# Performance work log

Measured on AMD Instinct MI355X. Metric: run time of the kernel, lower is better.

Reference implementation:

```python
import jax, jax.numpy as jnp
import numpy as np

N_ATOMS = 8192
N_PAIR = 131072
F = 128
N_HEAD = 8
FH = F // N_HEAD            # 16
DEGREES = [1, 2, 3]
N_DEG = len(DEGREES)
REPEATS = np.array([2 * l + 1 for l in DEGREES])  # [3,5,7]
M_TOT = int(REPEATS.sum())  # 15
K_RBF = 32
H_FILT = 64
FILT_OUT = 2 * N_DEG * F    # 768


def setup_inputs() -> dict:
    key = jax.random.key(0)
    ks = jax.random.split(key, 12)
    x = jax.random.normal(ks[0], (N_ATOMS, F), dtype=jnp.float32)
    rbf_ij = jax.random.uniform(ks[1], (N_PAIR, K_RBF), dtype=jnp.float32)
    sph_ij = jax.random.normal(ks[2], (N_PAIR, M_TOT), dtype=jnp.float32)
    phi_r_cut = jax.random.uniform(ks[3], (N_PAIR,), dtype=jnp.float32)
    idx_i = jnp.sort(jax.random.randint(ks[4], (N_PAIR,), 0, N_ATOMS))
    idx_j = jax.random.randint(ks[5], (N_PAIR,), 0, N_ATOMS)
    pair_mask = jnp.ones((N_PAIR,), dtype=jnp.float32)
    # params (lecun-normal-ish scaling)
    W_Q = jax.random.normal(ks[6], (N_DEG, N_HEAD, FH, FH), dtype=jnp.float32) / np.sqrt(FH)
    W_K = jax.random.normal(ks[7], (N_DEG, N_HEAD, FH, FH), dtype=jnp.float32) / np.sqrt(FH)
    a = jax.random.normal(ks[8], (N_DEG, N_HEAD, 2 * FH), dtype=jnp.float32) / np.sqrt(2 * FH)
    mlp_w1 = jax.random.normal(ks[9], (K_RBF, H_FILT), dtype=jnp.float32) / np.sqrt(K_RBF)
    mlp_b1 = jnp.zeros((H_FILT,), dtype=jnp.float32)
    mlp_w2 = jax.random.normal(ks[10], (H_FILT, FILT_OUT), dtype=jnp.float32) / np.sqrt(H_FILT)
    mlp_b2 = jnp.zeros((FILT_OUT,), dtype=jnp.float32)
    return {"x": x, "rbf_ij": rbf_ij, "sph_ij": sph_ij, "phi_r_cut": phi_r_cut,
            "idx_i": idx_i, "idx_j": idx_j, "pair_mask": pair_mask,
            "W_Q": W_Q, "W_K": W_K, "a": a,
            "mlp_w1": mlp_w1, "mlp_b1": mlp_b1, "mlp_w2": mlp_w2, "mlp_b2": mlp_b2}


def reference(x, rbf_ij, sph_ij, phi_r_cut, idx_i, idx_j, pair_mask,
              W_Q, W_K, a, mlp_w1, mlp_b1, mlp_w2, mlp_b2):
    n = x.shape[0]
    x_head = x.reshape(n, N_HEAD, FH)                       # (n, h, fh)
    # per-atom, per-degree, per-head linear maps
    Q = jnp.einsum('dhij,nhj->ndhi', W_Q, x_head)           # (n, d, h, fh)
    K = jnp.einsum('dhij,nhj->ndhi', W_K, x_head)
    m4 = pair_mask[:, None, None, None]
    Q_i = Q[idx_i] * m4                                     # (p, d, h, fh)
    K_j = K[idx_j] * m4
    QK = jnp.concatenate((Q_i, K_j), axis=-1)               # (p, d, h, 2fh)
    # radial filter MLP
    h1 = jax.nn.silu(rbf_ij @ mlp_w1 + mlp_b1)
    W_ij = (h1 @ mlp_w2 + mlp_b2).reshape(-1, N_DEG, N_HEAD, 2 * FH)
    W_ij = W_ij * phi_r_cut[:, None, None, None]
    # attention logits (non-softmax)
    alpha = jnp.sum(QK * W_ij * a[None], axis=-1)           # (p, d, h)
    alpha = jnp.repeat(alpha, REPEATS, axis=1, total_repeat_length=M_TOT)  # (p, m, h)
    alpha = alpha / jnp.sqrt(jnp.float32(FH))               # att_scale
    # outer product with spherical harmonics + scatter
    x_j = x_head[idx_j] * pair_mask[:, None, None]          # (p, h, fh)
    z = alpha[..., None] * (sph_ij[:, :, None, None] * x_j[:, None, :, :])  # (p, m, h, fh)
    z = z.reshape(z.shape[0], M_TOT, F)                     # (p, m, F)
    return jax.ops.segment_sum(z, idx_i, num_segments=n)    # (n, m, F)
```

## Files before the change

### kernel.cpp

```cpp
#include <hip/hip_runtime.h>
#include <hip/hip_bf16.h>

#define N_ATOMS 8192
#define N_PAIR  131072
#define F       128
#define N_HEAD  8
#define FH      16
#define N_DEG   3
#define M_TOT   15
#define K_RBF   32
#define H_FILT  64
#define FILT_OUT 768
#define NDH     24
#define ATB     4

typedef __attribute__((ext_vector_type(8))) unsigned short u16x8;

__device__ __forceinline__ float bf2f(unsigned short u) {
    return __uint_as_float(((unsigned)u) << 16);
}
__device__ __forceinline__ unsigned short f2bfbits(float f) {
    __hip_bfloat16 b = __float2bfloat16(f);
    return *reinterpret_cast<unsigned short*>(&b);
}

__global__ void k_seg(const int* __restrict__ idx_i, int* __restrict__ row_start) {
    int p = blockIdx.x * 256 + threadIdx.x;
    if (p >= N_PAIR) return;
    int ii = idx_i[p];
    int prev = (p == 0) ? -1 : idx_i[p - 1];
    for (int a = prev + 1; a <= ii; ++a) row_start[a] = p;
    if (p == N_PAIR - 1) {
        for (int a = ii + 1; a <= N_ATOMS; ++a) row_start[a] = N_PAIR;
    }
}

__global__ void k_zero(int* __restrict__ counts, int* __restrict__ cnt2) {
    int t = blockIdx.x * 256 + threadIdx.x;
    if (t < N_ATOMS) { counts[t] = 0; cnt2[t] = 0; }
}

__global__ void k_hist(const int* __restrict__ idx_j, int* __restrict__ counts) {
    int p = blockIdx.x * 256 + threadIdx.x;
    if (p < N_PAIR) atomicAdd(&counts[idx_j[p]], 1);
}

__global__ __launch_bounds__(1024) void k_scan(const int* __restrict__ counts,
                                               int* __restrict__ offsets) {
    __shared__ int ts[1024];
    int tid = threadIdx.x;
    int base = tid * 8;
    int v[8]; int tot = 0;
    #pragma unroll
    for (int q = 0; q < 8; ++q) { v[q] = counts[base + q]; tot += v[q]; }
    ts[tid] = tot; __syncthreads();
    for (int off = 1; off < 1024; off <<= 1) {
        int t2 = (tid >= off) ? ts[tid - off] : 0;
        __syncthreads();
        ts[tid] += t2;
        __syncthreads();
    }
    int excl = ts[tid] - tot;
    #pragma unroll
    for (int q = 0; q < 8; ++q) { offsets[base + q] = excl; excl += v[q]; }
    if (tid == 1023) offsets[N_ATOMS] = ts[1023];
}

__global__ void k_place(const int* __restrict__ idx_j, const int* __restrict__ offsets,
                        int* __restrict__ cnt2, int* __restrict__ sorted,
                        int* __restrict__ rank) {
    int p = blockIdx.x * 256 + threadIdx.x;
    if (p < N_PAIR) {
        int j = idx_j[p];
        int pos = offsets[j] + atomicAdd(&cnt2[j], 1);
        sorted[pos] = p;
        rank[p] = pos;
    }
}

__global__ __launch_bounds__(256) void k_wc(
    const float* __restrict__ WQ, const float* __restrict__ WK,
    const float* __restrict__ avec, const float* __restrict__ W2,
    const float* __restrict__ b2,
    float* __restrict__ Wc, float* __restrict__ bc)
{
    int bx = blockIdx.x;
    int side = bx / NDH, dh = bx % NDH;
    int d = dh >> 3, h = dh & 7;
    int colbase = d * 256 + h * 32 + side * 16;
    const float* W = (side == 0) ? WQ : WK;
    __shared__ float w2s[64][16];
    __shared__ float ws[16][16];
    __shared__ float as[16];
    __shared__ float b2s[16];
    int tid = threadIdx.x;
    for (int e = tid; e < 64 * 16; e += 256)
        w2s[e >> 4][e & 15] = W2[(e >> 4) * FILT_OUT + colbase + (e & 15)];
    if (tid < 16 * 16) ws[tid >> 4][tid & 15] = W[((d * 8 + h) * 16) * 16 + tid];
    if (tid < 16) { as[tid] = avec[dh * 32 + side * 16 + tid]; b2s[tid] = b2[colbase + tid]; }
    __syncthreads();
    for (int o = tid; o < 64 * 16; o += 256) {
        int k = o >> 4, j = o & 15;
        float s = 0.f;
        #pragma unroll
        for (int c = 0; c < 16; ++c) s += w2s[k][c] * as[c] * ws[c][j];
        Wc[((size_t)bx * 64 + k) * 16 + j] = s;
    }
    if (tid < 16) {
        float s = 0.f;
        #pragma unroll
        for (int c = 0; c < 16; ++c) s += b2s[c] * as[c] * ws[c][tid];
        bc[bx * 16 + tid] = s;
    }
}

__global__ __launch_bounds__(256) void k_gfused(
    const float* __restrict__ x, const float* __restrict__ Wc,
    const float* __restrict__ bc,
    __hip_bfloat16* __restrict__ Gq, __hip_bfloat16* __restrict__ Gk,
    float* __restrict__ bq, float* __restrict__ bk)
{
    int bx = blockIdx.x;
    int by = blockIdx.y;
    int side = by / NDH, dh = by % NDH;
    int h = dh & 7;
    int n0 = bx * 64;
    __shared__ float xh[64][17];
    __shared__ float bcs[16];
    int tid = threadIdx.x;
    for (int e = tid; e < 64 * 16; e += 256)
        xh[e >> 4][e & 15] = x[(size_t)(n0 + (e >> 4)) * F + h * 16 + (e & 15)];
    if (tid < 16) bcs[tid] = bc[by * 16 + tid];
    int k = tid & 63, wv = tid >> 6;
    float wcr[16];
    const float* wp = Wc + ((size_t)by * 64 + k) * 16;
    #pragma unroll
    for (int j = 0; j < 16; ++j) wcr[j] = wp[j];
    __syncthreads();
    __hip_bfloat16* G = (side == 0) ? Gq : Gk;
    #pragma unroll 4
    for (int it = 0; it < 16; ++it) {
        int at = wv * 16 + it;
        float acc = 0.f;
        #pragma unroll
        for (int j = 0; j < 16; ++j) acc += wcr[j] * xh[at][j];
        G[(size_t)(n0 + at) * 1536 + dh * 64 + k] = __float2bfloat16(acc);
    }
    if (tid < 64) {
        float* B = (side == 0) ? bq : bk;
        float s = 0.f;
        #pragma unroll
        for (int j = 0; j < 16; ++j) s += bcs[j] * xh[tid][j];
        B[(n0 + tid) * NDH + dh] = s;
    }
}

__global__ __launch_bounds__(256) void k_h1(
    const float* __restrict__ rbf, const float* __restrict__ W1,
    const float* __restrict__ b1, unsigned short* __restrict__ h1)
{
    __shared__ float w1s[K_RBF][H_FILT];
    __shared__ float b1s[H_FILT];
    __shared__ float rbfs[64][33];
    int tid = threadIdx.x;
    int p0 = blockIdx.x * 64;
    for (int e = tid; e < K_RBF * H_FILT; e += 256) w1s[e >> 6][e & 63] = W1[e];
    if (tid < H_FILT) b1s[tid] = b1[tid];
    for (int e = tid; e < 64 * K_RBF; e += 256)
        rbfs[e >> 5][e & 31] = rbf[(size_t)p0 * K_RBF + e];
    __syncthreads();
    int pp = tid >> 2;
    int kbase = (tid & 3) * 16;
    float acc[16];
    #pragma unroll
    for (int q = 0; q < 16; ++q) acc[q] = b1s[kbase + q];
    for (int c = 0; c < K_RBF; ++c) {
        float r = rbfs[pp][c];
        #pragma unroll
        for (int q = 0; q < 16; ++q) acc[q] += r * w1s[c][kbase + q];
    }
    u16x8 o0, o1;
    #pragma unroll
    for (int q = 0; q < 8; ++q) {
        float s0 = acc[q];     o0[q] = f2bfbits(s0 / (1.f + __expf(-s0)));
        float s1 = acc[q + 8]; o1[q] = f2bfbits(s1 / (1.f + __expf(-s1)));
    }
    unsigned short* hp = h1 + (size_t)(p0 + pp) * 64 + kbase;
    *reinterpret_cast<u16x8*>(hp) = o0;
    *reinterpret_cast<u16x8*>(hp + 8) = o1;
}

__global__ __launch_bounds__(256) void k_alphak2(
    const int* __restrict__ sorted, const int* __restrict__ idx_j,
    const unsigned short* __restrict__ h1,
    const __hip_bfloat16* __restrict__ Gk, const float* __restrict__ bk,
    unsigned short* __restrict__ alphaKs)
{
    __shared__ unsigned short h1s[64][64];
    __shared__ float als[64][24];
    __shared__ int ps[64];
    __shared__ int js[64];
    int tid = threadIdx.x;
    int c0 = blockIdx.x * 64;
    if (tid < 64) {
        int pid = sorted[c0 + tid];
        ps[tid] = pid;
        js[tid] = idx_j[pid];
    }
    __syncthreads();
    for (int e = tid; e < 64 * 8; e += 256) {
        int slot = e >> 3, seg = e & 7;
        *reinterpret_cast<u16x8*>(&h1s[slot][seg * 8]) =
            *reinterpret_cast<const u16x8*>(h1 + (size_t)ps[slot] * 64 + seg * 8);
    }
    __syncthreads();
    const unsigned short* GkU = reinterpret_cast<const unsigned short*>(Gk);
    int seg = tid & 7;
    #pragma unroll 4
    for (int t = 0; t < 48; ++t) {
        int task = t * 256 + tid;
        int dhslot = task >> 3;
        int slot = dhslot / 24;
        int dh = dhslot - slot * 24;
        const unsigned short* g = GkU + (size_t)js[slot] * 1536 + dh * 64 + seg * 8;
        u16x8 gv = *reinterpret_cast<const u16x8*>(g);
        u16x8 hv = *reinterpret_cast<const u16x8*>(&h1s[slot][seg * 8]);
        float p = 0.f;
        #pragma unroll
        for (int v = 0; v < 8; ++v) p += bf2f(gv[v]) * bf2f(hv[v]);
        p += __shfl_xor(p, 1);
        p += __shfl_xor(p, 2);
        p += __shfl_xor(p, 4);
        if (seg == 0) als[slot][dh] = p;
    }
    __syncthreads();
    for (int e = tid; e < 64 * 24; e += 256) {
        int slot = e / 24, dh = e - slot * 24;
        float val = als[slot][dh] + bk[js[slot] * NDH + dh];
        alphaKs[(size_t)c0 * 24 + e] = f2bfbits(val);
    }
}

__global__ __launch_bounds__(256) void k_alphaA2(
    const int* __restrict__ idx_i, const int* __restrict__ rank,
    const float* __restrict__ phi, const float* __restrict__ mask,
    const unsigned short* __restrict__ h1,
    const __hip_bfloat16* __restrict__ Gq, const float* __restrict__ bq,
    const unsigned short* __restrict__ alphaKs,
    float* __restrict__ alphaF)
{
    __shared__ unsigned short h1s[64][64];
    __shared__ float als[64][24];
    __shared__ int is[64];
    __shared__ int rks[64];
    __shared__ float pms[64];
    int tid = threadIdx.x;
    int p0 = blockIdx.x * 64;
    if (tid < 64) {
        int p = p0 + tid;
        is[tid] = idx_i[p];
        rks[tid] = rank[p];
        pms[tid] = phi[p] * mask[p] * 0.25f;
    }
    __syncthreads();
    for (int e = tid; e < 64 * 8; e += 256) {
        int slot = e >> 3, seg = e & 7;
        *reinterpret_cast<u16x8*>(&h1s[slot][seg * 8]) =
            *reinterpret_cast<const u16x8*>(h1 + (size_t)(p0 + slot) * 64 + seg * 8);
    }
    __syncthreads();
    const unsigned short* GqU = reinterpret_cast<const unsigned short*>(Gq);
    int seg = tid & 7;
    #pragma unroll 4
    for (int t = 0; t < 48; ++t) {
        int task = t * 256 + tid;
        int dhslot = task >> 3;
        int slot = dhslot / 24;
        int dh = dhslot - slot * 24;
        const unsigned short* g = GqU + (size_t)is[slot] * 1536 + dh * 64 + seg * 8;
        u16x8 gv = *reinterpret_cast<const u16x8*>(g);
        u16x8 hv = *reinterpret_cast<const u16x8*>(&h1s[slot][seg * 8]);
        float p = 0.f;
        #pragma unroll
        for (int v = 0; v < 8; ++v) p += bf2f(gv[v]) * bf2f(hv[v]);
        p += __shfl_xor(p, 1);
        p += __shfl_xor(p, 2);
        p += __shfl_xor(p, 4);
        if (seg == 0) als[slot][dh] = p;
    }
    __syncthreads();
    for (int e = tid; e < 64 * 24; e += 256) {
        int slot = e / 24, dh = e - slot * 24;
        float val = als[slot][dh] + bq[is[slot] * NDH + dh]
                  + bf2f(alphaKs[(size_t)rks[slot] * 24 + dh]);
        alphaF[(size_t)p0 * 24 + e] = val * pms[slot];
    }
}

__global__ __launch_bounds__(256) void k_aggr4(
    const float* __restrict__ x, const float* __restrict__ sph,
    const float* __restrict__ mask,
    const int* __restrict__ idx_i, const int* __restrict__ idx_j,
    const float* __restrict__ alphaF,
    const int* __restrict__ row_start, float* __restrict__ out)
{
    int a0 = blockIdx.x * ATB;
    int tid = threadIdx.x;
    int f = tid & 127, grp = tid >> 7, h = f >> 4;

    __shared__ float xls[32][128];
    __shared__ float als[32][24];
    __shared__ float sls[32][15];
    __shared__ int   iis[32];
    __shared__ int   jjs[32];
    __shared__ float xms[32];
    __shared__ int   rs[ATB + 1];

    if (tid <= ATB) rs[tid] = row_start[a0 + tid];
    __syncthreads();
    int pstart = rs[0], pend = rs[ATB];

    float acc[8];
    #pragma unroll
    for (int m = 0; m < 8; ++m) acc[m] = 0.f;
    int cur = -1;

    for (int pc = pstart; pc < pend; pc += 32) {
        int nb = min(32, pend - pc);
        __syncthreads();
        if (tid < nb) {
            int p = pc + tid;
            iis[tid] = idx_i[p];
            jjs[tid] = idx_j[p];
            xms[tid] = mask[p];
        }
        for (int e = tid; e < nb * 24; e += 256)
            als[e / 24][e % 24] = alphaF[(size_t)pc * 24 + e];
        for (int e = tid; e < nb * 15; e += 256)
            sls[e / 15][e % 15] = sph[(size_t)pc * 15 + e];
        __syncthreads();
        for (int e = tid; e < nb * 32; e += 256) {
            int q = e >> 5, c4 = e & 31;
            float4 v = *reinterpret_cast<const float4*>(x + (size_t)jjs[q] * F + c4 * 4);
            float m_ = xms[q];
            v.x *= m_; v.y *= m_; v.z *= m_; v.w *= m_;
            *reinterpret_cast<float4*>(&xls[q][c4 * 4]) = v;
        }
        __syncthreads();
        for (int q = 0; q < nb; ++q) {
            int ia = iis[q];
            if (ia != cur) {
                if (cur >= 0) {
                    size_t ob = (size_t)cur * (M_TOT * F) + f;
                    if (grp == 0) {
                        #pragma unroll
                        for (int m = 0; m < 8; ++m) out[ob + m * 128] = acc[m];
                    } else {
                        #pragma unroll
                        for (int m = 0; m < 7; ++m) out[ob + (8 + m) * 128] = acc[m];
                    }
                }
                cur = ia;
                #pragma unroll
                for (int m = 0; m < 8; ++m) acc[m] = 0.f;
            }
            float xv = xls[q][f];
            if (grp == 0) {
                float t0 = als[q][h] * xv;
                float t1 = als[q][8 + h] * xv;
                acc[0] += t0 * sls[q][0];
                acc[1] += t0 * sls[q][1];
                acc[2] += t0 * sls[q][2];
                #pragma unroll
                for (int m = 3; m < 8; ++m) acc[m] += t1 * sls[q][m];
            } else {
                float t2 = als[q][16 + h] * xv;
                #pragma unroll
                for (int m = 0; m < 7; ++m) acc[m] += t2 * sls[q][8 + m];
            }
        }
    }
    if (cur >= 0) {
        size_t ob = (size_t)cur * (M_TOT * F) + f;
        if (grp == 0) {
            #pragma unroll
            for (int m = 0; m < 8; ++m) out[ob + m * 128] = acc[m];
        } else {
            #pragma unroll
            for (int m = 0; m < 7; ++m) out[ob + (8 + m) * 128] = acc[m];
        }
    }
    for (int a = 0; a < ATB; ++a) {
        if (rs[a] == rs[a + 1]) {
            size_t ob = (size_t)(a0 + a) * (M_TOT * F) + f;
            if (grp == 0) {
                #pragma unroll
                for (int m = 0; m < 8; ++m) out[ob + m * 128] = 0.f;
            } else {
                #pragma unroll
                for (int m = 0; m < 7; ++m) out[ob + (8 + m) * 128] = 0.f;
            }
        }
    }
}

extern "C" void kernel_launch(void* const* d_in, const int* in_sizes, int n_in,
                              void* d_out, int out_size, void* d_ws, size_t ws_size,
                              hipStream_t stream) {
    const float* x     = (const float*)d_in[0];
    const float* rbf   = (const float*)d_in[1];
    const float* sph   = (const float*)d_in[2];
    const float* phi   = (const float*)d_in[3];
    const int*   idx_i = (const int*)d_in[4];
    const int*   idx_j = (const int*)d_in[5];
    const float* mask  = (const float*)d_in[6];
    const float* WQ    = (const float*)d_in[7];
    const float* WK    = (const float*)d_in[8];
    const float* av    = (const float*)d_in[9];
    const float* W1    = (const float*)d_in[10];
    const float* b1    = (const float*)d_in[11];
    const float* W2    = (const float*)d_in[12];
    const float* b2    = (const float*)d_in[13];
    float* out = (float*)d_out;
    char* ws = (char*)d_ws;

    __hip_bfloat16* Gq = (__hip_bfloat16*)(ws + 0);
    __hip_bfloat16* Gk = (__hip_bfloat16*)(ws + 25165824);
    float* alphaF = (float*)(ws + 25165824);
    float* bq = (float*)(ws + 50331648);
    float* bk = (float*)(ws + 51118080);
    int* row_start = (int*)(ws + 51904512);
    int* counts    = (int*)(ws + 51937792);
    int* offsets   = (int*)(ws + 51970560);
    int* cnt2      = (int*)(ws + 52003840);
    int* sorted    = (int*)(ws + 52036608);
    int* rank      = (int*)(ws + 52560896);
    unsigned short* h1      = (unsigned short*)(ws + 53085184);
    unsigned short* alphaKs = (unsigned short*)(ws + 69862400);
    float* Wc = (float*)(ws + 76153856);
    float* bc = (float*)(ws + 76350464);

    k_zero<<<(N_ATOMS + 255) / 256, 256, 0, stream>>>(counts, cnt2);
    k_seg<<<(N_PAIR + 255) / 256, 256, 0, stream>>>(idx_i, row_start);
    k_hist<<<(N_PAIR + 255) / 256, 256, 0, stream>>>(idx_j, counts);
    k_scan<<<1, 1024, 0, stream>>>(counts, offsets);
    k_place<<<(N_PAIR + 255) / 256, 256, 0, stream>>>(idx_j, offsets, cnt2, sorted, rank);
    k_wc<<<48, 256, 0, stream>>>(WQ, WK, av, W2, b2, Wc, bc);
    k_gfused<<<dim3(N_ATOMS / 64, 48), 256, 0, stream>>>(x, Wc, bc, Gq, Gk, bq, bk);
    k_h1<<<N_PAIR / 64, 256, 0, stream>>>(rbf, W1, b1, h1);
    k_alphak2<<<N_PAIR / 64, 256, 0, stream>>>(sorted, idx_j, h1, Gk, bk, alphaKs);
    k_alphaA2<<<N_PAIR / 64, 256, 0, stream>>>(idx_i, rank, phi, mask, h1, Gq, bq,
                                               alphaKs, alphaF);
    k_aggr4<<<N_ATOMS / ATB, 256, 0, stream>>>(x, sph, mask, idx_i, idx_j, alphaF,
                                               row_start, out);
}
```

Baseline: 208.6 us.

## Fuse query-side alpha computation into aggregation kernel with shared Gq tile

Merges the query-side attention-logit kernel into the per-atom aggregation kernel. Each block stages its 4 atoms' Gq rows in shared memory, computes alpha per pair chunk in-block, and so drops the alphaF round trip through global memory and one launch. It also stops staging x rows in shared memory and instead loads x values directly four pairs at a time. The cost is more shared memory per block and extra compute serialized inside the aggregation loop, which may lower occupancy.

```diff
diff --git a/kernel.cpp b/kernel.cpp
--- a/kernel.cpp
+++ b/kernel.cpp
@@ -196,7 +196,7 @@
     const __hip_bfloat16* __restrict__ Gk, const float* __restrict__ bk,
     unsigned short* __restrict__ alphaKs)
 {
-    __shared__ unsigned short h1s[64][64];
+    __shared__ __align__(16) unsigned short h1s[64][64];
     __shared__ float als[64][24];
     __shared__ int ps[64];
     __shared__ int js[64];
@@ -241,82 +241,40 @@
     }
 }
 
-__global__ __launch_bounds__(256) void k_alphaA2(
-    const int* __restrict__ idx_i, const int* __restrict__ rank,
+__global__ __launch_bounds__(256) void k_aggrF(
+    const float* __restrict__ x, const float* __restrict__ sph,
     const float* __restrict__ phi, const float* __restrict__ mask,
+    const int* __restrict__ idx_i, const int* __restrict__ idx_j,
+    const int* __restrict__ rank,
     const unsigned short* __restrict__ h1,
     const __hip_bfloat16* __restrict__ Gq, const float* __restrict__ bq,
     const unsigned short* __restrict__ alphaKs,
-    float* __restrict__ alphaF)
-{
-    __shared__ unsigned short h1s[64][64];
-    __shared__ float als[64][24];
-    __shared__ int is[64];
-    __shared__ int rks[64];
-    __shared__ float pms[64];
-    int tid = threadIdx.x;
-    int p0 = blockIdx.x * 64;
-    if (tid < 64) {
-        int p = p0 + tid;
-        is[tid] = idx_i[p];
-        rks[tid] = rank[p];
-        pms[tid] = phi[p] * mask[p] * 0.25f;
-    }
-    __syncthreads();
-    for (int e = tid; e < 64 * 8; e += 256) {
-        int slot = e >> 3, seg = e & 7;
-        *reinterpret_cast<u16x8*>(&h1s[slot][seg * 8]) =
-            *reinterpret_cast<const u16x8*>(h1 + (size_t)(p0 + slot) * 64 + seg * 8);
-    }
-    __syncthreads();
-    const unsigned short* GqU = reinterpret_cast<const unsigned short*>(Gq);
-    int seg = tid & 7;
-    #pragma unroll 4
-    for (int t = 0; t < 48; ++t) {
-        int task = t * 256 + tid;
-        int dhslot = task >> 3;
-        int slot = dhslot / 24;
-        int dh = dhslot - slot * 24;
-        const unsigned short* g = GqU + (size_t)is[slot] * 1536 + dh * 64 + seg * 8;
-        u16x8 gv = *reinterpret_cast<const u16x8*>(g);
-        u16x8 hv = *reinterpret_cast<const u16x8*>(&h1s[slot][seg * 8]);
-        float p = 0.f;
-        #pragma unroll
-        for (int v = 0; v < 8; ++v) p += bf2f(gv[v]) * bf2f(hv[v]);
-        p += __shfl_xor(p, 1);
-        p += __shfl_xor(p, 2);
-        p += __shfl_xor(p, 4);
-        if (seg == 0) als[slot][dh] = p;
-    }
-    __syncthreads();
-    for (int e = tid; e < 64 * 24; e += 256) {
-        int slot = e / 24, dh = e - slot * 24;
-        float val = als[slot][dh] + bq[is[slot] * NDH + dh]
-                  + bf2f(alphaKs[(size_t)rks[slot] * 24 + dh]);
-        alphaF[(size_t)p0 * 24 + e] = val * pms[slot];
-    }
-}
-
-__global__ __launch_bounds__(256) void k_aggr4(
-    const float* __restrict__ x, const float* __restrict__ sph,
-    const float* __restrict__ mask,
-    const int* __restrict__ idx_i, const int* __restrict__ idx_j,
-    const float* __restrict__ alphaF,
     const int* __restrict__ row_start, float* __restrict__ out)
 {
     int a0 = blockIdx.x * ATB;
     int tid = threadIdx.x;
     int f = tid & 127, grp = tid >> 7, h = f >> 4;
 
-    __shared__ float xls[32][128];
+    __shared__ __align__(16) unsigned short gqs[ATB][1536];
+    __shared__ __align__(16) unsigned short h1s[32][72];
+    __shared__ __align__(16) unsigned short aksS[32][24];
+    __shared__ float sls[32][16];
     __shared__ float als[32][24];
-    __shared__ float sls[32][15];
+    __shared__ float bqs[ATB][24];
     __shared__ int   iis[32];
     __shared__ int   jjs[32];
-    __shared__ float xms[32];
+    __shared__ float pms[32];
     __shared__ int   rs[ATB + 1];
 
     if (tid <= ATB) rs[tid] = row_start[a0 + tid];
+    {
+        const u16x8* g0 = reinterpret_cast<const u16x8*>(
+            reinterpret_cast<const unsigned short*>(Gq) + (size_t)a0 * 1536);
+        u16x8* gd = reinterpret_cast<u16x8*>(&gqs[0][0]);
+        for (int e = tid; e < ATB * 192; e += 256) gd[e] = g0[e];
+    }
+    for (int e = tid; e < ATB * 24; e += 256)
+        bqs[e / 24][e % 24] = bq[(a0 + e / 24) * NDH + (e % 24)];
     __syncthreads();
     int pstart = rs[0], pend = rs[ATB];
 
@@ -324,6 +282,38 @@
     #pragma unroll
     for (int m = 0; m < 8; ++m) acc[m] = 0.f;
     int cur = -1;
+
+#define FLUSH(CUR)                                                        \
+    { size_t ob = (size_t)(CUR) * (M_TOT * F) + f;                        \
+      if (grp == 0) {                                                     \
+          _Pragma("unroll")                                               \
+          for (int m = 0; m < 8; ++m) out[ob + m * 128] = acc[m];         \
+      } else {                                                            \
+          _Pragma("unroll")                                               \
+          for (int m = 0; m < 7; ++m) out[ob + (8 + m) * 128] = acc[m];   \
+      } }
+
+#define AGG_STEP(Q, XV)                                                   \
+    { int ia = iis[Q];                                                    \
+      if (ia != cur) {                                                    \
+          if (cur >= 0) FLUSH(cur);                                       \
+          cur = ia;                                                       \
+          _Pragma("unroll")                                               \
+          for (int m = 0; m < 8; ++m) acc[m] = 0.f;                       \
+      }                                                                   \
+      if (grp == 0) {                                                     \
+          float t0 = als[Q][h] * (XV);                                    \
+          float t1 = als[Q][8 + h] * (XV);                                \
+          acc[0] += t0 * sls[Q][0];                                       \
+          acc[1] += t0 * sls[Q][1];                                       \
+          acc[2] += t0 * sls[Q][2];                                       \
+          _Pragma("unroll")                                               \
+          for (int m = 3; m < 8; ++m) acc[m] += t1 * sls[Q][m];           \
+      } else {                                                            \
+          float t2 = als[Q][16 + h] * (XV);                               \
+          _Pragma("unroll")                                               \
+          for (int m = 0; m < 7; ++m) acc[m] += t2 * sls[Q][8 + m];       \
+      } }
 
     for (int pc = pstart; pc < pend; pc += 32) {
         int nb = min(32, pend - pc);
@@ -332,64 +322,60 @@
             int p = pc + tid;
             iis[tid] = idx_i[p];
             jjs[tid] = idx_j[p];
-            xms[tid] = mask[p];
-        }
-        for (int e = tid; e < nb * 24; e += 256)
-            als[e / 24][e % 24] = alphaF[(size_t)pc * 24 + e];
+            float mk = mask[p];
+            pms[tid] = phi[p] * mk * mk * 0.25f;
+        }
+        for (int e = tid; e < nb * 8; e += 256) {
+            int slot = e >> 3, seg = e & 7;
+            *reinterpret_cast<u16x8*>(&h1s[slot][seg * 8]) =
+                *reinterpret_cast<const u16x8*>(h1 + (size_t)(pc + slot) * 64 + seg * 8);
+        }
+        for (int e = tid; e < nb * 3; e += 256) {
+            int slot = e / 3, part = e - slot * 3;
+            int rk = rank[pc + slot];
+            *reinterpret_cast<u16x8*>(&aksS[slot][part * 8]) =
+                *reinterpret_cast<const u16x8*>(alphaKs + (size_t)rk * 24 + part * 8);
+        }
         for (int e = tid; e < nb * 15; e += 256)
             sls[e / 15][e % 15] = sph[(size_t)pc * 15 + e];
         __syncthreads();
-        for (int e = tid; e < nb * 32; e += 256) {
-            int q = e >> 5, c4 = e & 31;
-            float4 v = *reinterpret_cast<const float4*>(x + (size_t)jjs[q] * F + c4 * 4);
-            float m_ = xms[q];
-            v.x *= m_; v.y *= m_; v.z *= m_; v.w *= m_;
-            *reinterpret_cast<float4*>(&xls[q][c4 * 4]) = v;
+        {
+            int seg = tid & 7;
+            #pragma unroll 4
+            for (int t = 0; t < 24; ++t) {
+                int task = t * 256 + tid;
+                if (task < nb * 192) {
+                    int dhslot = task >> 3;
+                    int slot = dhslot / 24;
+                    int dh = dhslot - slot * 24;
+                    int ai = iis[slot] - a0;
+                    u16x8 gv = *reinterpret_cast<const u16x8*>(&gqs[ai][dh * 64 + seg * 8]);
+                    u16x8 hv = *reinterpret_cast<const u16x8*>(&h1s[slot][seg * 8]);
+                    float pp = 0.f;
+                    #pragma unroll
+                    for (int v = 0; v < 8; ++v) pp += bf2f(gv[v]) * bf2f(hv[v]);
+                    pp += __shfl_xor(pp, 1);
+                    pp += __shfl_xor(pp, 2);
+                    pp += __shfl_xor(pp, 4);
+                    if (seg == 0)
+                        als[slot][dh] = (pp + bqs[ai][dh] + bf2f(aksS[slot][dh])) * pms[slot];
+                }
+            }
         }
         __syncthreads();
-        for (int q = 0; q < nb; ++q) {
-            int ia = iis[q];
-            if (ia != cur) {
-                if (cur >= 0) {
-                    size_t ob = (size_t)cur * (M_TOT * F) + f;
-                    if (grp == 0) {
-                        #pragma unroll
-                        for (int m = 0; m < 8; ++m) out[ob + m * 128] = acc[m];
-                    } else {
-                        #pragma unroll
-                        for (int m = 0; m < 7; ++m) out[ob + (8 + m) * 128] = acc[m];
-                    }
-                }
-                cur = ia;
-                #pragma unroll
-                for (int m = 0; m < 8; ++m) acc[m] = 0.f;
-            }
-            float xv = xls[q][f];
-            if (grp == 0) {
-                float t0 = als[q][h] * xv;
-                float t1 = als[q][8 + h] * xv;
-                acc[0] += t0 * sls[q][0];
-                acc[1] += t0 * sls[q][1];
-                acc[2] += t0 * sls[q][2];
-                #pragma unroll
-                for (int m = 3; m < 8; ++m) acc[m] += t1 * sls[q][m];
-            } else {
-                float t2 = als[q][16 + h] * xv;
-                #pragma unroll
-                for (int m = 0; m < 7; ++m) acc[m] += t2 * sls[q][8 + m];
-            }
-        }
-    }
-    if (cur >= 0) {
-        size_t ob = (size_t)cur * (M_TOT * F) + f;
-        if (grp == 0) {
-            #pragma unroll
-            for (int m = 0; m < 8; ++m) out[ob + m * 128] = acc[m];
-        } else {
-            #pragma unroll
-            for (int m = 0; m < 7; ++m) out[ob + (8 + m) * 128] = acc[m];
-        }
-    }
+        for (int qg = 0; qg < nb; qg += 4) {
+            int n4 = nb - qg;
+            float xa = x[(size_t)jjs[qg] * F + f];
+            float xb = (n4 > 1) ? x[(size_t)jjs[qg + 1] * F + f] : 0.f;
+            float xc = (n4 > 2) ? x[(size_t)jjs[qg + 2] * F + f] : 0.f;
+            float xd = (n4 > 3) ? x[(size_t)jjs[qg + 3] * F + f] : 0.f;
+            AGG_STEP(qg, xa);
+            if (n4 > 1) AGG_STEP(qg + 1, xb);
+            if (n4 > 2) AGG_STEP(qg + 2, xc);
+            if (n4 > 3) AGG_STEP(qg + 3, xd);
+        }
+    }
+    if (cur >= 0) FLUSH(cur);
     for (int a = 0; a < ATB; ++a) {
         if (rs[a] == rs[a + 1]) {
             size_t ob = (size_t)(a0 + a) * (M_TOT * F) + f;
@@ -402,6 +388,8 @@
             }
         }
     }
+#undef AGG_STEP
+#undef FLUSH
 }
 
 extern "C" void kernel_launch(void* const* d_in, const int* in_sizes, int n_in,
@@ -426,7 +414,6 @@
 
     __hip_bfloat16* Gq = (__hip_bfloat16*)(ws + 0);
     __hip_bfloat16* Gk = (__hip_bfloat16*)(ws + 25165824);
-    float* alphaF = (float*)(ws + 25165824);
     float* bq = (float*)(ws + 50331648);
     float* bk = (float*)(ws + 51118080);
     int* row_start = (int*)(ws + 51904512);
@@ -449,8 +436,6 @@
     k_gfused<<<dim3(N_ATOMS / 64, 48), 256, 0, stream>>>(x, Wc, bc, Gq, Gk, bq, bk);
     k_h1<<<N_PAIR / 64, 256, 0, stream>>>(rbf, W1, b1, h1);
     k_alphak2<<<N_PAIR / 64, 256, 0, stream>>>(sorted, idx_j, h1, Gk, bk, alphaKs);
-    k_alphaA2<<<N_PAIR / 64, 256, 0, stream>>>(idx_i, rank, phi, mask, h1, Gq, bq,
-                                               alphaKs, alphaF);
-    k_aggr4<<<N_ATOMS / ATB, 256, 0, stream>>>(x, sph, mask, idx_i, idx_j, alphaF,
-                                               row_start, out);
-}
+    k_aggrF<<<N_ATOMS / ATB, 256, 0, stream>>>(x, sph, phi, mask, idx_i, idx_j, rank,
+                                               h1, Gq, bq, alphaKs, row_start, out);
+}
```

Measured after the change: 220.1 us. 1.06x slower.
